# Optimization experiments

Measured on AMD Instinct MI355X. Metric: run time of the kernel, lower is better.

## Reference

```python
import jax, jax.numpy as jnp
import numpy as np

T, B, IN, H, OUT, K = 1024, 128, 32, 512, 32, 64


def frac_weights(d):
    # d: [H] per-channel fractional differencing order (= 0.5*sigmoid(b_d)).
    # pi_j = pi_{j-1} * (j-1-d)/j, pi_0 = 1 (coeffs of (1-B)^d expansion).
    # Returned layout matches torch get_ws: index 0 -> lag K, index K-1 -> lag 1.
    j = jnp.arange(1, K + 1, dtype=d.dtype)[:, None]          # [K,1]
    pi = jnp.cumprod((j - 1.0 - d[None, :]) / j, axis=0)       # [K,H], pi[j-1]=coeff lag j
    return pi[::-1]                                            # [K,H]


def frac_filter(x, pi):
    # x: [T,B,H]; pi: [K,H] (lag K..1). Computes x_tilde[t] = x[t] + sum_j pi_j x[t-j]
    # (zero history before t=0, matching a zero-initialized memory buffer)
    # via a causal depthwise convolution.
    Hc = pi.shape[1]
    kern = jnp.concatenate([pi, jnp.ones((1, Hc), pi.dtype)], axis=0)  # [K+1,H]
    kern = kern.T[:, None, :]                                          # [H,1,K+1]
    xb = x.transpose(1, 2, 0)                                          # [B,H,T]
    y = jax.lax.conv_general_dilated(
        xb, kern, window_strides=(1,), padding=[(K, 0)],
        dimension_numbers=("NCH", "OIH", "NCH"), feature_group_count=Hc)
    return y.transpose(2, 0, 1)                                        # [T,B,H]


def rnn_layer(x, W_ih, b_ih, W_hh, b_hh, W_ho, b_ho, pi):
    # MRNNFixDCell over full sequence: fractional-differencing filter on the
    # layer input, then tanh RNN recurrence, then linear readout per step.
    xt = frac_filter(x, pi)
    pre = jnp.einsum('tbi,hi->tbh', xt, W_ih) + b_ih + b_hh   # input part precomputed

    def step(h, p):
        h = jnp.tanh(p + h @ W_hh.T)
        return h, h

    h0 = jnp.zeros((x.shape[1], W_hh.shape[0]), x.dtype)
    _, hs = jax.lax.scan(step, h0, pre)                        # [T,B,H]
    return jnp.einsum('tbh,oh->tbo', hs, W_ho) + b_ho          # [T,B,out]


def setup_inputs() -> dict:
    key = jax.random.key(0)
    ks = jax.random.split(key, 10)
    s = 0.05
    return {
        "inputs": jax.random.normal(ks[0], (T, B, IN), jnp.float32),
        "b_d":   jax.random.normal(ks[1], (1, H), jnp.float32) * 0.1,
        "W_emb": jax.random.normal(ks[2], (H, IN), jnp.float32) * s,
        "b_emb": jnp.zeros((H,), jnp.float32),
        "W_ih0": jax.random.normal(ks[3], (H, H), jnp.float32) * s,
        "b_ih0": jnp.zeros((H,), jnp.float32),
        "W_hh0": jax.random.normal(ks[4], (H, H), jnp.float32) * s,
        "b_hh0": jnp.zeros((H,), jnp.float32),
        "W_ho0": jax.random.normal(ks[5], (H, H), jnp.float32) * s,
        "b_ho0": jnp.zeros((H,), jnp.float32),
        "W_ih1": jax.random.normal(ks[6], (H, H), jnp.float32) * s,
        "b_ih1": jnp.zeros((H,), jnp.float32),
        "W_hh1": jax.random.normal(ks[7], (H, H), jnp.float32) * s,
        "b_hh1": jnp.zeros((H,), jnp.float32),
        "W_ho1": jax.random.normal(ks[8], (OUT, H), jnp.float32) * s,
        "b_ho1": jnp.zeros((OUT,), jnp.float32),
    }


def reference(inputs, b_d, W_emb, b_emb,
              W_ih0, b_ih0, W_hh0, b_hh0, W_ho0, b_ho0,
              W_ih1, b_ih1, W_hh1, b_hh1, W_ho1, b_ho1):
    x = jnp.einsum('tbi,hi->tbh', inputs, W_emb) + b_emb       # input embedding
    d = 0.5 * jax.nn.sigmoid(b_d)[0]                           # [H], fixed d per channel
    pi = frac_weights(d)                                       # [K,H]
    y0 = rnn_layer(x,  W_ih0, b_ih0, W_hh0, b_hh0, W_ho0, b_ho0, pi)
    y1 = rnn_layer(y0, W_ih1, b_ih1, W_hh1, b_hh1, W_ho1, b_ho1, pi)
    return y1[-1]                                              # last-step output [B,OUT]
```

## Files before the change

### kernel.cpp

```cpp
#include <hip/hip_runtime.h>
#include <hip/hip_bf16.h>

#define Tn 1024
#define Bn 128
#define INn 32
#define Hn 512
#define OUTn 32
#define Kn 64
#define LPAD 536

typedef __attribute__((ext_vector_type(8))) __bf16 bf16x8;
typedef __attribute__((ext_vector_type(4))) float f32x4;
typedef __attribute__((ext_vector_type(4))) unsigned int u32x4;
typedef __attribute__((ext_vector_type(2))) unsigned int u32x2;

typedef const __attribute__((address_space(1))) void* gas_p;
typedef __attribute__((address_space(3))) void* las_p;

static __device__ __forceinline__ float bf2f(unsigned short u) {
    union { unsigned int i; float f; } c; c.i = ((unsigned int)u) << 16; return c.f;
}
static __device__ __forceinline__ unsigned short f2bf(float f) {
    union { float f; unsigned int i; } c; c.f = f;
    unsigned int x = c.i;
    return (unsigned short)((x + 0x7fffu + ((x >> 16) & 1u)) >> 16);
}
static __device__ __forceinline__ float tanh_fast(float x) {
    float xc = fminf(fmaxf(x, -10.f), 10.f);
    float e = __expf(2.f * xc);
    return (e - 1.f) * __builtin_amdgcn_rcpf(e + 1.f);
}

__global__ __launch_bounds__(256) void cvt_k(const float* __restrict__ in,
                                             unsigned short* __restrict__ out, int n4) {
    int i = blockIdx.x * 256 + threadIdx.x;
    if (i < n4) {
        float4 v = ((const float4*)in)[i];
        ushort4 o;
        o.x = f2bf(v.x); o.y = f2bf(v.y); o.z = f2bf(v.z); o.w = f2bf(v.w);
        ((ushort4*)out)[i] = o;
    }
}

__global__ __launch_bounds__(512) void prep_small(const float* __restrict__ b_d,
                                                  const float* __restrict__ bih0, const float* __restrict__ bhh0,
                                                  const float* __restrict__ bih1, const float* __restrict__ bhh1,
                                                  float* __restrict__ pi, float* __restrict__ bias0,
                                                  float* __restrict__ bias1) {
    int i = threadIdx.x;
    float d = 0.5f / (1.0f + expf(-b_d[i]));
    float c = 1.0f;
    for (int j = 1; j <= Kn; ++j) {
        c *= ((float)(j - 1) - d) / (float)j;
        pi[(j - 1) * Hn + i] = c;
    }
    bias0[i] = bih0[i] + bhh0[i];
    bias1[i] = bih1[i] + bhh1[i];
}

__global__ __launch_bounds__(256, 2) void gemm_bt(const unsigned short* __restrict__ A,
                                                  const unsigned short* __restrict__ Bm,
                                                  unsigned short* __restrict__ C,
                                                  const float* __restrict__ bias,
                                                  int M, int N, int K) {
    __shared__ unsigned short As[128 * 32];
    __shared__ unsigned short Bs[128 * 32];
    int ntile = N >> 7;
    int bm = blockIdx.x / ntile;
    int bn = blockIdx.x - bm * ntile;
    size_t m0 = (size_t)bm << 7;
    int n0 = bn << 7;
    int tid = threadIdx.x;
    int lane = tid & 63, w = tid >> 6;
    int wm = w >> 1, wn = w & 1;
    int r = lane & 15, g = lane >> 4;
    int srow = tid >> 2, sblk = tid & 3;
    f32x4 acc[4][4] = {};
    for (int k0 = 0; k0 < K; k0 += 32) {
#pragma unroll
        for (int it = 0; it < 2; ++it) {
            const unsigned short* ga = A + (m0 + it * 64 + srow) * (size_t)K + k0 + sblk * 8;
            __builtin_amdgcn_global_load_lds((gas_p)ga, (las_p)((char*)As + it * 4096 + w * 1024), 16, 0, 0);
            const unsigned short* gbp = Bm + ((size_t)(n0 + it * 64 + srow)) * (size_t)K + k0 + sblk * 8;
            __builtin_amdgcn_global_load_lds((gas_p)gbp, (las_p)((char*)Bs + it * 4096 + w * 1024), 16, 0, 0);
        }
        __syncthreads();
        bf16x8 af[4], bfr[4];
#pragma unroll
        for (int m = 0; m < 4; ++m) af[m] = *(const bf16x8*)&As[(wm * 64 + m * 16 + r) * 32 + g * 8];
#pragma unroll
        for (int n = 0; n < 4; ++n) bfr[n] = *(const bf16x8*)&Bs[(wn * 64 + n * 16 + r) * 32 + g * 8];
#pragma unroll
        for (int m = 0; m < 4; ++m)
#pragma unroll
            for (int n = 0; n < 4; ++n)
                acc[m][n] = __builtin_amdgcn_mfma_f32_16x16x32_bf16(af[m], bfr[n], acc[m][n], 0, 0, 0);
        __syncthreads();
    }
#pragma unroll
    for (int n = 0; n < 4; ++n) {
        int col = n0 + wn * 64 + n * 16 + r;
        float bv = bias[col];
#pragma unroll
        for (int m = 0; m < 4; ++m) {
            size_t row0 = m0 + wm * 64 + m * 16 + g * 4;
#pragma unroll
            for (int q = 0; q < 4; ++q)
                C[(row0 + q) * (size_t)N + col] = f2bf(acc[m][n][q] + bv);
        }
    }
}

__global__ __launch_bounds__(256, 2) void filt_k(const unsigned short* __restrict__ X,
                                                 const float* __restrict__ Pi,
                                                 unsigned short* __restrict__ Y, int t_off) {
    int tid = threadIdx.x;
    int il = tid & 63, ts = tid >> 6;
    int i = blockIdx.x * 64 + il;
    int b = blockIdx.z;
    int tbase = t_off + blockIdx.y * 128 + ts * 32;
    float xr[96];
#pragma unroll
    for (int k2 = 0; k2 < 96; ++k2) {
        int t = tbase - 64 + k2;
        xr[k2] = (t >= 0) ? bf2f(X[(size_t)t * (Bn * Hn) + b * Hn + i]) : 0.0f;
    }
    float acc[32];
#pragma unroll
    for (int tt = 0; tt < 32; ++tt) acc[tt] = xr[64 + tt];
#pragma unroll
    for (int j = 1; j <= 64; ++j) {
        float p = Pi[(j - 1) * Hn + i];
#pragma unroll
        for (int tt = 0; tt < 32; ++tt) acc[tt] += p * xr[64 + tt - j];
    }
#pragma unroll
    for (int tt = 0; tt < 32; ++tt)
        Y[(size_t)(tbase - t_off + tt) * (Bn * Hn) + b * Hn + i] = f2bf(acc[tt]);
}

#define MFMA8(K0)                                                                              \
    {                                                                                          \
        _Pragma("unroll") for (int kk = 0; kk < 8; ++kk) {                                     \
            bf16x8 bf = *(const bf16x8*)(hrow + (K0 + kk) * 32 + g * 8);                       \
            acc0 = __builtin_amdgcn_mfma_f32_16x16x32_bf16(wreg0[K0 + kk], bf, acc0, 0, 0, 0); \
            acc1 = __builtin_amdgcn_mfma_f32_16x16x32_bf16(wreg1[K0 + kk], bf, acc1, 0, 0, 0); \
        }                                                                                      \
    }

__global__ __launch_bounds__(512, 1) void rec14_k(const unsigned short* __restrict__ W,
                                                  const unsigned short* pre,
                                                  unsigned short* hs,
                                                  float* __restrict__ hfin,
                                                  unsigned int* ex, int fbase) {
    __shared__ unsigned short hl[2][16][LPAD];
    int bid = blockIdx.x;
    int gb = bid & 7, go = bid >> 3;
    int tid = threadIdx.x, lane = tid & 63, w = tid >> 6;
    int r = lane & 15, g = lane >> 4;
    int ob = go * 256 + w * 32;
    bf16x8 wreg0[16], wreg1[16];
#pragma unroll
    for (int kk = 0; kk < 16; ++kk) {
        wreg0[kk] = *(const bf16x8*)(W + (size_t)(ob + r) * Hn + kk * 32 + g * 8);
        wreg1[kk] = *(const bf16x8*)(W + (size_t)(ob + 16 + r) * Hn + kk * 32 + g * 8);
    }
    int bb = gb * 16 + r;
    const unsigned short* preP = pre + (size_t)bb * Hn + ob + g * 4;
    unsigned short* hsP = hs ? hs + (size_t)bb * Hn + ob + g * 4 : (unsigned short*)0;
    int myblk = gb * 2 + go, pblk = gb * 2 + (go ^ 1);
    int pbatch = tid >> 5;
    int pcol = (go ^ 1) * 256 + (tid & 31) * 8;
    unsigned long long pfA0 = *(const unsigned long long*)(preP);
    unsigned long long pfA1 = *(const unsigned long long*)(preP + 16);
    unsigned long long pfB0 = *(const unsigned long long*)(preP + (size_t)(Bn * Hn));
    unsigned long long pfB1 = *(const unsigned long long*)(preP + (size_t)(Bn * Hn) + 16);

#define REC_STEP(TT, P0, P1, ISLAST)                                                             \
    {                                                                                            \
        asm volatile("s_waitcnt lgkmcnt(0)\n\ts_barrier" ::: "memory");   \
        f32x4 acc0 = {0.f, 0.f, 0.f, 0.f}, acc1 = {0.f, 0.f, 0.f, 0.f};                          \
        const unsigned short* hrow = &hl[TT & 1][r][0];                                          \
        if (TT > 0) {                                                                            \
            if (go == 0) MFMA8(0) else MFMA8(8)                           \
            unsigned tg = (unsigned)(fbase + TT);                                                \
            const unsigned int* pp = ex + ((size_t)(TT & 1) * 16 + pblk) * 4096 + tid * 8;       \
            u32x4 a, b;                                                                          \
            while (1) {                                                                          \
                asm volatile("global_load_dwordx4 %0, %2, off sc1\n\t"                           \
                             "global_load_dwordx4 %1, %2, off offset:16 sc1\n\t"                 \
                             "s_waitcnt vmcnt(0)"                                                \
                             : "=v"(a), "=v"(b) : "v"(pp) : "memory");                           \
                bool ok = (a.x & 0xffffu) == tg && (a.y & 0xffffu) == tg &&                      \
                          (a.z & 0xffffu) == tg && (a.w & 0xffffu) == tg &&                      \
                          (b.x & 0xffffu) == tg && (b.y & 0xffffu) == tg &&                      \
                          (b.z & 0xffffu) == tg && (b.w & 0xffffu) == tg;                        \
                if (ok) break;                                                                   \
            }                                                                                    \
            unsigned int* ld = (unsigned int*)&hl[TT & 1][pbatch][pcol];                         \
            ld[0] = (a.x >> 16) | (a.y & 0xffff0000u);                                           \
            ld[1] = (a.z >> 16) | (a.w & 0xffff0000u);                                           \
            ld[2] = (b.x >> 16) | (b.y & 0xffff0000u);                                           \
            ld[3] = (b.z >> 16) | (b.w & 0xffff0000u);                                           \
        }                                                                                        \
                \
        int tn = (TT + 2 < Tn) ? TT + 2 : Tn - 1;                                                \
        unsigned long long n0 = *(const unsigned long long*)(preP + (size_t)tn * (Bn * Hn));     \
        unsigned long long n1 = *(const unsigned long long*)(preP + (size_t)tn * (Bn * Hn) + 16);\
        asm volatile("s_waitcnt lgkmcnt(0)\n\ts_barrier" ::: "memory");    \
        if (TT > 0) {                                                                            \
            if (go == 0) MFMA8(8) else MFMA8(0)                       \
        }                                                                                        \
        union { unsigned long long u; unsigned short s[4]; } p0, p1;                             \
        p0.u = P0; p1.u = P1;                                                                    \
        float h0 = tanh_fast(acc0[0] + bf2f(p0.s[0]));                                           \
        float h1 = tanh_fast(acc0[1] + bf2f(p0.s[1]));                                           \
        float h2 = tanh_fast(acc0[2] + bf2f(p0.s[2]));                                           \
        float h3 = tanh_fast(acc0[3] + bf2f(p0.s[3]));                                           \
        float h4 = tanh_fast(acc1[0] + bf2f(p1.s[0]));                                           \
        float h5 = tanh_fast(acc1[1] + bf2f(p1.s[1]));                                           \
        float h6 = tanh_fast(acc1[2] + bf2f(p1.s[2]));                                           \
        float h7 = tanh_fast(acc1[3] + bf2f(p1.s[3]));                                           \
        unsigned int b0 = f2bf(h0), b1 = f2bf(h1), b2 = f2bf(h2), b3 = f2bf(h3);                 \
        unsigned int b4 = f2bf(h4), b5 = f2bf(h5), b6 = f2bf(h6), b7 = f2bf(h7);                 \
        unsigned tv = (unsigned)(fbase + TT + 1);                                                \
        u32x4 s0 = { (b0 << 16) | tv, (b1 << 16) | tv, (b2 << 16) | tv, (b3 << 16) | tv };       \
        u32x4 s1 = { (b4 << 16) | tv, (b5 << 16) | tv, (b6 << 16) | tv, (b7 << 16) | tv };       \
        unsigned int* wp = ex + ((size_t)((TT + 1) & 1) * 16 + myblk) * 4096 + r * 256 + w * 32 + g * 4; \
        asm volatile("global_store_dwordx4 %0, %1, off sc1\n\t"                                  \
                     "global_store_dwordx4 %0, %2, off offset:64 sc1"                            \
                     :: "v"(wp), "v"(s0), "v"(s1) : "memory");                                   \
        {                                                                                        \
            u32x2 v0 = { b0 | (b1 << 16), b2 | (b3 << 16) };                                     \
            u32x2 v1 = { b4 | (b5 << 16), b6 | (b7 << 16) };                                     \
            *(u32x2*)&hl[(TT + 1) & 1][r][ob + g * 4] = v0;                                      \
            *(u32x2*)&hl[(TT + 1) & 1][r][ob + 16 + g * 4] = v1;                                 \
        }                                                                                        \
        if (hsP) {                                                                               \
            union { unsigned int u[2]; unsigned long long v; } o0, o1;                           \
            o0.u[0] = b0 | (b1 << 16); o0.u[1] = b2 | (b3 << 16);                                \
            o1.u[0] = b4 | (b5 << 16); o1.u[1] = b6 | (b7 << 16);                                \
            *(unsigned long long*)(hsP + (size_t)TT * (Bn * Hn)) = o0.v;                         \
            *(unsigned long long*)(hsP + (size_t)TT * (Bn * Hn) + 16) = o1.v;                    \
        }                                                                                        \
        if (ISLAST && hfin) {                                                                    \
            float* hf = hfin + (size_t)bb * Hn + ob + g * 4;                                     \
            hf[0] = h0; hf[1] = h1; hf[2] = h2; hf[3] = h3;                                      \
            hf[16] = h4; hf[17] = h5; hf[18] = h6; hf[19] = h7;                                  \
        }                                                                                        \
        P0 = n0; P1 = n1;                                                                        \
    }

    for (int t = 0; t < Tn; t += 2) {
        REC_STEP(t, pfA0, pfA1, false)
        REC_STEP((t + 1), pfB0, pfB1, (t + 1 == Tn - 1))
    }
#undef REC_STEP
}

__global__ __launch_bounds__(64) void readout_k(const float* __restrict__ hfin,
                                                const float* __restrict__ Who1,
                                                const float* __restrict__ bho1,
                                                float* __restrict__ out) {
    int b = blockIdx.x;
    __shared__ float hv[Hn];
    int tid = threadIdx.x;
    for (int i = tid; i < Hn; i += 64) hv[i] = hfin[(size_t)b * Hn + i];
    __syncthreads();
    if (tid < OUTn) {
        float acc = bho1[tid];
        const float* wrow = Who1 + (size_t)tid * Hn;
#pragma unroll 8
        for (int i = 0; i < Hn; ++i) acc += wrow[i] * hv[i];
        out[b * OUTn + tid] = acc;
    }
}

extern "C" void kernel_launch(void* const* d_in, const int* in_sizes, int n_in,
                              void* d_out, int out_size, void* d_ws, size_t ws_size,
                              hipStream_t stream) {
    const float* inputs = (const float*)d_in[0];
    const float* b_d    = (const float*)d_in[1];
    const float* W_emb  = (const float*)d_in[2];
    const float* b_emb  = (const float*)d_in[3];
    const float* W_ih0  = (const float*)d_in[4];
    const float* b_ih0  = (const float*)d_in[5];
    const float* W_hh0  = (const float*)d_in[6];
    const float* b_hh0  = (const float*)d_in[7];
    const float* W_ho0  = (const float*)d_in[8];
    const float* b_ho0  = (const float*)d_in[9];
    const float* W_ih1  = (const float*)d_in[10];
    const float* b_ih1  = (const float*)d_in[11];
    const float* W_hh1  = (const float*)d_in[12];
    const float* b_hh1  = (const float*)d_in[13];
    const float* W_ho1  = (const float*)d_in[14];
    const float* b_ho1  = (const float*)d_in[15];

    char* ws = (char*)d_ws;
    size_t off = 0;
    auto alloc = [&](size_t bytes) {
        void* p = ws + off;
        off += (bytes + 255) & ~(size_t)255;
        return p;
    };
    unsigned short* B    = (unsigned short*)alloc(134217728);
    unsigned short* Hf   = (unsigned short*)alloc(67108864);
    unsigned short* inb  = (unsigned short*)alloc(8388608);
    unsigned short* Wemb = (unsigned short*)alloc(32768);
    unsigned short* Wih0 = (unsigned short*)alloc(524288);
    unsigned short* Whh0 = (unsigned short*)alloc(524288);
    unsigned short* Who0 = (unsigned short*)alloc(524288);
    unsigned short* Wih1 = (unsigned short*)alloc(524288);
    unsigned short* Whh1 = (unsigned short*)alloc(524288);
    float* bias0 = (float*)alloc(2048);
    float* bias1 = (float*)alloc(2048);
    float* piB   = (float*)alloc(131072);
    unsigned int* ex = (unsigned int*)alloc(524288);
    float* hfin = (float*)alloc(262144);
    (void)ws_size; (void)in_sizes; (void)n_in; (void)out_size;

    unsigned short* B_hi = B + (size_t)512 * Bn * Hn;
    const size_t halfBytes = 67108864;
    const int Mh = 512 * Bn;

    hipMemsetAsync(ex, 0, 524288, stream);
    cvt_k<<<4096, 256, 0, stream>>>(inputs, inb, 1048576);
    cvt_k<<<16,   256, 0, stream>>>(W_emb, Wemb, 4096);
    cvt_k<<<256,  256, 0, stream>>>(W_ih0, Wih0, 65536);
    cvt_k<<<256,  256, 0, stream>>>(W_hh0, Whh0, 65536);
    cvt_k<<<256,  256, 0, stream>>>(W_ho0, Who0, 65536);
    cvt_k<<<256,  256, 0, stream>>>(W_ih1, Wih1, 65536);
    cvt_k<<<256,  256, 0, stream>>>(W_hh1, Whh1, 65536);
    prep_small<<<1, 512, 0, stream>>>(b_d, b_ih0, b_hh0, b_ih1, b_hh1, piB, bias0, bias1);

    gemm_bt<<<4096, 256, 0, stream>>>(inb, Wemb, B, b_emb, Tn * Bn, Hn, INn);
    filt_k<<<dim3(8, 4, 128), 256, 0, stream>>>(B, piB, Hf, 512);
    gemm_bt<<<2048, 256, 0, stream>>>(Hf, Wih0, B_hi, bias0, Mh, Hn, Hn);
    filt_k<<<dim3(8, 4, 128), 256, 0, stream>>>(B, piB, Hf, 0);
    gemm_bt<<<2048, 256, 0, stream>>>(Hf, Wih0, B, bias0, Mh, Hn, Hn);
    rec14_k<<<16, 512, 0, stream>>>(Whh0, B, B, nullptr, ex, 0);
    gemm_bt<<<2048, 256, 0, stream>>>(B_hi, Who0, Hf, b_ho0, Mh, Hn, Hn);
    hipMemcpyAsync(B_hi, Hf, halfBytes, hipMemcpyDeviceToDevice, stream);
    gemm_bt<<<2048, 256, 0, stream>>>(B, Who0, Hf, b_ho0, Mh, Hn, Hn);
    hipMemcpyAsync(B, Hf, halfBytes, hipMemcpyDeviceToDevice, stream);
    filt_k<<<dim3(8, 4, 128), 256, 0, stream>>>(B, piB, Hf, 512);
    gemm_bt<<<2048, 256, 0, stream>>>(Hf, Wih1, B_hi, bias1, Mh, Hn, Hn);
    filt_k<<<dim3(8, 4, 128), 256, 0, stream>>>(B, piB, Hf, 0);
    gemm_bt<<<2048, 256, 0, stream>>>(Hf, Wih1, B, bias1, Mh, Hn, Hn);
    rec14_k<<<16, 512, 0, stream>>>(Whh1, B, nullptr, hfin, ex, 1024);
    readout_k<<<128, 64, 0, stream>>>(hfin, W_ho1, b_ho1, (float*)d_out);
}
```

Measured before the change: 5.588 ms.

## Split recurrence across 32 blocks with LDS-resident weights and per-lane global h exchange

After: 13.80 ms. +146.9%, slower.

```diff
diff --git a/kernel.cpp b/kernel.cpp
--- a/kernel.cpp
+++ b/kernel.cpp
@@ -7,12 +7,10 @@
 #define Hn 512
 #define OUTn 32
 #define Kn 64
-#define LPAD 536
 
 typedef __attribute__((ext_vector_type(8))) __bf16 bf16x8;
 typedef __attribute__((ext_vector_type(4))) float f32x4;
 typedef __attribute__((ext_vector_type(4))) unsigned int u32x4;
-typedef __attribute__((ext_vector_type(2))) unsigned int u32x2;
 
 typedef const __attribute__((address_space(1))) void* gas_p;
 typedef __attribute__((address_space(3))) void* las_p;
@@ -139,78 +137,109 @@
         Y[(size_t)(tbase - t_off + tt) * (Bn * Hn) + b * Hn + i] = f2bf(acc[tt]);
 }
 
-#define MFMA8(K0)                                                                              \
-    {                                                                                          \
-        _Pragma("unroll") for (int kk = 0; kk < 8; ++kk) {                                     \
-            bf16x8 bf = *(const bf16x8*)(hrow + (K0 + kk) * 32 + g * 8);                       \
-            acc0 = __builtin_amdgcn_mfma_f32_16x16x32_bf16(wreg0[K0 + kk], bf, acc0, 0, 0, 0); \
-            acc1 = __builtin_amdgcn_mfma_f32_16x16x32_bf16(wreg1[K0 + kk], bf, acc1, 0, 0, 0); \
-        }                                                                                      \
-    }
-
-__global__ __launch_bounds__(512, 1) void rec14_k(const unsigned short* __restrict__ W,
+__global__ __launch_bounds__(256, 1) void rec16_k(const unsigned short* __restrict__ W,
                                                   const unsigned short* pre,
                                                   unsigned short* hs,
                                                   float* __restrict__ hfin,
                                                   unsigned int* ex, int fbase) {
-    __shared__ unsigned short hl[2][16][LPAD];
+    __shared__ unsigned short Wl[128 * 512];
     int bid = blockIdx.x;
-    int gb = bid & 7, go = bid >> 3;
+    int gb = bid & 7, oq = bid >> 3;
     int tid = threadIdx.x, lane = tid & 63, w = tid >> 6;
     int r = lane & 15, g = lane >> 4;
-    int ob = go * 256 + w * 32;
-    bf16x8 wreg0[16], wreg1[16];
-#pragma unroll
-    for (int kk = 0; kk < 16; ++kk) {
-        wreg0[kk] = *(const bf16x8*)(W + (size_t)(ob + r) * Hn + kk * 32 + g * 8);
-        wreg1[kk] = *(const bf16x8*)(W + (size_t)(ob + 16 + r) * Hn + kk * 32 + g * 8);
+    int rx = r & 7;
+    int lr0 = w * 32 + r, lr1 = w * 32 + 16 + r;
+    int ob0 = oq * 128 + w * 32;
+#pragma unroll
+    for (int it = 0; it < 32; ++it) {
+        int row = it * 4 + w;
+        const unsigned short* gsrc = W + (size_t)(oq * 128 + row) * Hn + (size_t)((lane ^ (row & 7)) * 8);
+        __builtin_amdgcn_global_load_lds((gas_p)gsrc, (las_p)((char*)Wl + row * 1024), 16, 0, 0);
     }
     int bb = gb * 16 + r;
-    const unsigned short* preP = pre + (size_t)bb * Hn + ob + g * 4;
-    unsigned short* hsP = hs ? hs + (size_t)bb * Hn + ob + g * 4 : (unsigned short*)0;
-    int myblk = gb * 2 + go, pblk = gb * 2 + (go ^ 1);
-    int pbatch = tid >> 5;
-    int pcol = (go ^ 1) * 256 + (tid & 31) * 8;
+    const unsigned short* preP = pre + (size_t)bb * Hn + ob0 + g * 4;
+    unsigned short* hsP = hs ? hs + (size_t)bb * Hn + ob0 + g * 4 : (unsigned short*)0;
+    __syncthreads();
     unsigned long long pfA0 = *(const unsigned long long*)(preP);
     unsigned long long pfA1 = *(const unsigned long long*)(preP + 16);
     unsigned long long pfB0 = *(const unsigned long long*)(preP + (size_t)(Bn * Hn));
     unsigned long long pfB1 = *(const unsigned long long*)(preP + (size_t)(Bn * Hn) + 16);
 
+#define PACK2(E, O) (((E) >> 16) | ((O) & 0xffff0000u))
+#define ISSUEB(Q0, Q1, Q2, Q3, O0, O1, O2, O3)                                                \
+    asm volatile("global_load_dwordx4 %0, %4, off offset:" #O0 " sc1\n\t"                     \
+                 "global_load_dwordx4 %1, %4, off offset:" #O1 " sc1\n\t"                     \
+                 "global_load_dwordx4 %2, %4, off offset:" #O2 " sc1\n\t"                     \
+                 "global_load_dwordx4 %3, %4, off offset:" #O3 " sc1"                         \
+                 : "=v"(Q0), "=v"(Q1), "=v"(Q2), "=v"(Q3) : "v"(vp) : "memory")
+#define CHKB(J, Q0, Q1, Q2, Q3)                                                               \
+    if (!(nd & (1u << J))) {                                                                  \
+        unsigned m_ = (Q0.x ^ tg) | (Q0.y ^ tg) | (Q0.z ^ tg) | (Q0.w ^ tg) |                 \
+                      (Q1.x ^ tg) | (Q1.y ^ tg) | (Q1.z ^ tg) | (Q1.w ^ tg) |                 \
+                      (Q2.x ^ tg) | (Q2.y ^ tg) | (Q2.z ^ tg) | (Q2.w ^ tg) |                 \
+                      (Q3.x ^ tg) | (Q3.y ^ tg) | (Q3.z ^ tg) | (Q3.w ^ tg);                  \
+        if (!(m_ & 0xffffu)) nd |= (1u << J);                                                 \
+    }
+#define FRAG(KK, QA, QB)                                                                      \
+    {                                                                                         \
+        union { unsigned int u[4]; bf16x8 v; } hb_;                                          \
+        hb_.u[0] = PACK2(QA.x, QA.y); hb_.u[1] = PACK2(QA.z, QA.w);                           \
+        hb_.u[2] = PACK2(QB.x, QB.y); hb_.u[3] = PACK2(QB.z, QB.w);                           \
+        bf16x8 wf0_ = *(const bf16x8*)&Wl[lr0 * 512 + ((((KK) * 4 + g) ^ rx) << 3)];          \
+        bf16x8 wf1_ = *(const bf16x8*)&Wl[lr1 * 512 + ((((KK) * 4 + g) ^ rx) << 3)];          \
+        acc0 = __builtin_amdgcn_mfma_f32_16x16x32_bf16(wf0_, hb_.v, acc0, 0, 0, 0);           \
+        acc1 = __builtin_amdgcn_mfma_f32_16x16x32_bf16(wf1_, hb_.v, acc1, 0, 0, 0);           \
+    }
+
 #define REC_STEP(TT, P0, P1, ISLAST)                                                             \
     {                                                                                            \
-        asm volatile("s_waitcnt lgkmcnt(0)\n\ts_barrier" ::: "memory");   \
+        const int p = TT & 1;                                                                    \
+        unsigned tg = (unsigned)(fbase + TT);                                                    \
         f32x4 acc0 = {0.f, 0.f, 0.f, 0.f}, acc1 = {0.f, 0.f, 0.f, 0.f};                          \
-        const unsigned short* hrow = &hl[TT & 1][r][0];                                          \
+        u32x4 q00, q01, q02, q03, q10, q11, q12, q13, q20, q21, q22, q23, q30, q31, q32, q33;    \
+        u32x4 q40, q41, q42, q43, q50, q51, q52, q53, q60, q61, q62, q63, q70, q71, q72, q73;    \
         if (TT > 0) {                                                                            \
-            if (go == 0) MFMA8(0) else MFMA8(8)                           \
-            unsigned tg = (unsigned)(fbase + TT);                                                \
-            const unsigned int* pp = ex + ((size_t)(TT & 1) * 16 + pblk) * 4096 + tid * 8;       \
-            u32x4 a, b;                                                                          \
-            while (1) {                                                                          \
-                asm volatile("global_load_dwordx4 %0, %2, off sc1\n\t"                           \
-                             "global_load_dwordx4 %1, %2, off offset:16 sc1\n\t"                 \
-                             "s_waitcnt vmcnt(0)"                                                \
-                             : "=v"(a), "=v"(b) : "v"(pp) : "memory");                           \
-                bool ok = (a.x & 0xffffu) == tg && (a.y & 0xffffu) == tg &&                      \
-                          (a.z & 0xffffu) == tg && (a.w & 0xffffu) == tg &&                      \
-                          (b.x & 0xffffu) == tg && (b.y & 0xffffu) == tg &&                      \
-                          (b.z & 0xffffu) == tg && (b.w & 0xffffu) == tg;                        \
-                if (ok) break;                                                                   \
+            const unsigned int* vp = ex + ((size_t)p * 8 + gb) * 8192 + r * 512 + g * 8;         \
+            ISSUEB(q00, q01, q02, q03, 0, 16, 128, 144);                                         \
+            ISSUEB(q10, q11, q12, q13, 256, 272, 384, 400);                                      \
+            ISSUEB(q20, q21, q22, q23, 512, 528, 640, 656);                                      \
+            ISSUEB(q30, q31, q32, q33, 768, 784, 896, 912);                                      \
+            ISSUEB(q40, q41, q42, q43, 1024, 1040, 1152, 1168);                                  \
+            ISSUEB(q50, q51, q52, q53, 1280, 1296, 1408, 1424);                                  \
+            ISSUEB(q60, q61, q62, q63, 1536, 1552, 1664, 1680);                                  \
+            ISSUEB(q70, q71, q72, q73, 1792, 1808, 1920, 1936);                                  \
+            unsigned done = 0;                                                                   \
+            while (done != 0xffu) {                                                              \
+                asm volatile("s_waitcnt vmcnt(0)" ::: "memory");                                 \
+                __builtin_amdgcn_sched_barrier(0);                                               \
+                unsigned nd = done;                                                              \
+                CHKB(0, q00, q01, q02, q03) CHKB(1, q10, q11, q12, q13)                          \
+                CHKB(2, q20, q21, q22, q23) CHKB(3, q30, q31, q32, q33)                          \
+                CHKB(4, q40, q41, q42, q43) CHKB(5, q50, q51, q52, q53)                          \
+                CHKB(6, q60, q61, q62, q63) CHKB(7, q70, q71, q72, q73)                          \
+                if (nd == done) __builtin_amdgcn_s_sleep(2);                                     \
+                if (nd != 0xffu) {                                                               \
+                    if (!(nd & 1u))   ISSUEB(q00, q01, q02, q03, 0, 16, 128, 144);               \
+                    if (!(nd & 2u))   ISSUEB(q10, q11, q12, q13, 256, 272, 384, 400);            \
+                    if (!(nd & 4u))   ISSUEB(q20, q21, q22, q23, 512, 528, 640, 656);            \
+                    if (!(nd & 8u))   ISSUEB(q30, q31, q32, q33, 768, 784, 896, 912);            \
+                    if (!(nd & 16u))  ISSUEB(q40, q41, q42, q43, 1024, 1040, 1152, 1168);        \
+                    if (!(nd & 32u))  ISSUEB(q50, q51, q52, q53, 1280, 1296, 1408, 1424);        \
+                    if (!(nd & 64u))  ISSUEB(q60, q61, q62, q63, 1536, 1552, 1664, 1680);        \
+                    if (!(nd & 128u)) ISSUEB(q70, q71, q72, q73, 1792, 1808, 1920, 1936);        \
+                }                                                                                \
+                done = nd;                                                                       \
             }                                                                                    \
-            unsigned int* ld = (unsigned int*)&hl[TT & 1][pbatch][pcol];                         \
-            ld[0] = (a.x >> 16) | (a.y & 0xffff0000u);                                           \
-            ld[1] = (a.z >> 16) | (a.w & 0xffff0000u);                                           \
-            ld[2] = (b.x >> 16) | (b.y & 0xffff0000u);                                           \
-            ld[3] = (b.z >> 16) | (b.w & 0xffff0000u);                                           \
+            __builtin_amdgcn_sched_barrier(0);                                                   \
+            FRAG(0, q00, q01)  FRAG(1, q02, q03)  FRAG(2, q10, q11)  FRAG(3, q12, q13)           \
+            FRAG(4, q20, q21)  FRAG(5, q22, q23)  FRAG(6, q30, q31)  FRAG(7, q32, q33)           \
+            FRAG(8, q40, q41)  FRAG(9, q42, q43)  FRAG(10, q50, q51) FRAG(11, q52, q53)          \
+            FRAG(12, q60, q61) FRAG(13, q62, q63) FRAG(14, q70, q71) FRAG(15, q72, q73)          \
         }                                                                                        \
                 \
         int tn = (TT + 2 < Tn) ? TT + 2 : Tn - 1;                                                \
         unsigned long long n0 = *(const unsigned long long*)(preP + (size_t)tn * (Bn * Hn));     \
         unsigned long long n1 = *(const unsigned long long*)(preP + (size_t)tn * (Bn * Hn) + 16);\
-        asm volatile("s_waitcnt lgkmcnt(0)\n\ts_barrier" ::: "memory");    \
-        if (TT > 0) {                                                                            \
-            if (go == 0) MFMA8(8) else MFMA8(0)                       \
-        }                                                                                        \
         union { unsigned long long u; unsigned short s[4]; } p0, p1;                             \
         p0.u = P0; p1.u = P1;                                                                    \
         float h0 = tanh_fast(acc0[0] + bf2f(p0.s[0]));                                           \
@@ -223,19 +252,13 @@
         float h7 = tanh_fast(acc1[3] + bf2f(p1.s[3]));                                           \
         unsigned int b0 = f2bf(h0), b1 = f2bf(h1), b2 = f2bf(h2), b3 = f2bf(h3);                 \
         unsigned int b4 = f2bf(h4), b5 = f2bf(h5), b6 = f2bf(h6), b7 = f2bf(h7);                 \
-        unsigned tv = (unsigned)(fbase + TT + 1);                                                \
+        unsigned tv = tg + 1u;                                                                   \
         u32x4 s0 = { (b0 << 16) | tv, (b1 << 16) | tv, (b2 << 16) | tv, (b3 << 16) | tv };       \
         u32x4 s1 = { (b4 << 16) | tv, (b5 << 16) | tv, (b6 << 16) | tv, (b7 << 16) | tv };       \
-        unsigned int* wp = ex + ((size_t)((TT + 1) & 1) * 16 + myblk) * 4096 + r * 256 + w * 32 + g * 4; \
+        unsigned int* wp = ex + ((size_t)((TT + 1) & 1) * 8 + gb) * 8192 + r * 512 + ob0 + g * 4;\
         asm volatile("global_store_dwordx4 %0, %1, off sc1\n\t"                                  \
                      "global_store_dwordx4 %0, %2, off offset:64 sc1"                            \
                      :: "v"(wp), "v"(s0), "v"(s1) : "memory");                                   \
-        {                                                                                        \
-            u32x2 v0 = { b0 | (b1 << 16), b2 | (b3 << 16) };                                     \
-            u32x2 v1 = { b4 | (b5 << 16), b6 | (b7 << 16) };                                     \
-            *(u32x2*)&hl[(TT + 1) & 1][r][ob + g * 4] = v0;                                      \
-            *(u32x2*)&hl[(TT + 1) & 1][r][ob + 16 + g * 4] = v1;                                 \
-        }                                                                                        \
         if (hsP) {                                                                               \
             union { unsigned int u[2]; unsigned long long v; } o0, o1;                           \
             o0.u[0] = b0 | (b1 << 16); o0.u[1] = b2 | (b3 << 16);                                \
@@ -244,7 +267,7 @@
             *(unsigned long long*)(hsP + (size_t)TT * (Bn * Hn) + 16) = o1.v;                    \
         }                                                                                        \
         if (ISLAST && hfin) {                                                                    \
-            float* hf = hfin + (size_t)bb * Hn + ob + g * 4;                                     \
+            float* hf = hfin + (size_t)bb * Hn + ob0 + g * 4;                                    \
             hf[0] = h0; hf[1] = h1; hf[2] = h2; hf[3] = h3;                                      \
             hf[16] = h4; hf[17] = h5; hf[18] = h6; hf[19] = h7;                                  \
         }                                                                                        \
@@ -256,6 +279,10 @@
         REC_STEP((t + 1), pfB0, pfB1, (t + 1 == Tn - 1))
     }
 #undef REC_STEP
+#undef FRAG
+#undef CHKB
+#undef ISSUEB
+#undef PACK2
 }
 
 __global__ __launch_bounds__(64) void readout_k(const float* __restrict__ hfin,
@@ -338,7 +365,7 @@
     gemm_bt<<<2048, 256, 0, stream>>>(Hf, Wih0, B_hi, bias0, Mh, Hn, Hn);
     filt_k<<<dim3(8, 4, 128), 256, 0, stream>>>(B, piB, Hf, 0);
     gemm_bt<<<2048, 256, 0, stream>>>(Hf, Wih0, B, bias0, Mh, Hn, Hn);
-    rec14_k<<<16, 512, 0, stream>>>(Whh0, B, B, nullptr, ex, 0);
+    rec16_k<<<32, 256, 0, stream>>>(Whh0, B, B, nullptr, ex, 0);
     gemm_bt<<<2048, 256, 0, stream>>>(B_hi, Who0, Hf, b_ho0, Mh, Hn, Hn);
     hipMemcpyAsync(B_hi, Hf, halfBytes, hipMemcpyDeviceToDevice, stream);
     gemm_bt<<<2048, 256, 0, stream>>>(B, Who0, Hf, b_ho0, Mh, Hn, Hn);
@@ -347,6 +374,6 @@
     gemm_bt<<<2048, 256, 0, stream>>>(Hf, Wih1, B_hi, bias1, Mh, Hn, Hn);
     filt_k<<<dim3(8, 4, 128), 256, 0, stream>>>(B, piB, Hf, 0);
     gemm_bt<<<2048, 256, 0, stream>>>(Hf, Wih1, B, bias1, Mh, Hn, Hn);
-    rec14_k<<<16, 512, 0, stream>>>(Whh1, B, nullptr, hfin, ex, 1024);
+    rec16_k<<<32, 256, 0, stream>>>(Whh1, B, nullptr, hfin, ex, 1024);
     readout_k<<<128, 64, 0, stream>>>(hfin, W_ho1, b_ho1, (float*)d_out);
 }
```
